# Optimization experiments

Measured on AMD Instinct MI355X. Metric: run time of the kernel, lower is better.

The kernel has to match this reference:

```python
import jax, jax.numpy as jnp
import numpy as np

K = 5          # init kwarg k: k-1 = 4 nearest neighbors used, randint over [0, k-2]
DIMS = 512     # init kwarg dims


def _pairwise_dist(X):
    # Faithful to find_k: euclidean distance matrix, computed via the
    # ||a||^2 + ||b||^2 - 2ab gram trick instead of the O(T) python loop.
    sq = jnp.sum(X * X, axis=1)
    d2 = sq[:, None] + sq[None, :] - 2.0 * (X @ X.T)
    return jnp.sqrt(jnp.maximum(d2, 0.0))


def _generate(min_samples, n_per, key):
    # SMOTE.generate: for each minority row, n_per synthetic samples, each
    # interpolated toward a uniformly chosen one of its k-1 nearest neighbors.
    T, d = min_samples.shape
    D = _pairwise_dist(min_samples)                       # [T, T]
    nbrs = jnp.argsort(D, axis=1)[:, 1:K]                 # [T, k-1], drop self
    k1, k2 = jax.random.split(key)
    choice = jax.random.randint(k1, (T, n_per), 0, K - 1)          # nn = randint(0, k-2)
    u = jax.random.uniform(k2, (T, n_per, 1), dtype=min_samples.dtype)  # uniform(0,1)
    nn_idx = jnp.take_along_axis(nbrs, choice, axis=1)    # [T, n_per]
    base = min_samples[:, None, :]                        # [T, 1, d]
    diff = min_samples[nn_idx] - base                     # [T, n_per, d]
    # populate() fills row-major (outer loop i, inner loop over N) -> reshape matches
    return (base + u * diff).reshape(T * n_per, d)


def setup_inputs() -> dict:
    key = jax.random.key(0)
    n_major, n_minor = 24576, 8192
    X = jax.random.normal(key, (n_major + n_minor, DIMS), dtype=jnp.float32)
    y = jnp.concatenate([jnp.zeros((n_major,), jnp.int32),
                         jnp.ones((n_minor,), jnp.int32)])
    return {"X": X, "y": y}


def reference(X, y):
    # forward: oversample every non-dominant class up to the dominant count.
    y_np = np.asarray(y)                       # labels are concrete constants
    occ = np.bincount(y_np)                    # == one_hot(y).sum(0)
    dom = int(occ.argmax())
    n_occ = int(occ[dom])
    key = jax.random.key(42)
    X_out = X
    y_out = y.astype(jnp.float32)
    for c in range(len(occ)):
        if c == dom:
            continue
        n_per = int((n_occ - int(occ[c])) * 100 / int(occ[c])) // 100  # int(N/100)
        if n_per <= 0:
            continue
        cand = X[y_np == c]
        key, sub = jax.random.split(key)
        xs = _generate(cand, n_per, sub)
        X_out = jnp.concatenate([X_out, xs], axis=0)
        y_out = jnp.concatenate([y_out, jnp.full((xs.shape[0],), float(c), jnp.float32)])
    return X_out, y_out
```

## Files before the change

kernel.cpp:

```cpp
#include <hip/hip_runtime.h>
#include <stdint.h>
#include <math.h>

#ifndef JAX_PARTITIONABLE
#define JAX_PARTITIONABLE 1
#endif

#define DIM    512
#define NTOT   32768
#define NMAJ   24576
#define NMIN   8192
#define NGEN   16384
#define XROWS  49152
#define Y_OFF  ((size_t)XROWS * DIM)

#define NSLICE 8
#define KSLICE 6
#define NCAND  (NSLICE * KSLICE)

#define WS_H       (NMIN)
#define WS_L       (WS_H + NMIN * DIM / 2)
#define WS_CAND_F  (WS_L + NMIN * DIM / 2)
#define WS_NBR_F   (WS_CAND_F + NMIN * NCAND / 2)

typedef __attribute__((ext_vector_type(8))) short bfv8;
typedef __attribute__((ext_vector_type(4))) float f32x4;

__device__ __forceinline__ void tf2x32(uint32_t k0, uint32_t k1,
                                       uint32_t x0, uint32_t x1,
                                       uint32_t &o0, uint32_t &o1) {
  const uint32_t ks2 = k0 ^ k1 ^ 0x1BD11BDAu;
  x0 += k0; x1 += k1;
#define TF_R(r) { x0 += x1; x1 = (x1 << (r)) | (x1 >> (32 - (r))); x1 ^= x0; }
  TF_R(13) TF_R(15) TF_R(26) TF_R(6)
  x0 += k1;  x1 += ks2 + 1u;
  TF_R(17) TF_R(29) TF_R(16) TF_R(24)
  x0 += ks2; x1 += k0 + 2u;
  TF_R(13) TF_R(15) TF_R(26) TF_R(6)
  x0 += k0;  x1 += k1 + 3u;
  TF_R(17) TF_R(29) TF_R(16) TF_R(24)
  x0 += k1;  x1 += ks2 + 4u;
  TF_R(13) TF_R(15) TF_R(26) TF_R(6)
  x0 += ks2; x1 += k0 + 5u;
#undef TF_R
  o0 = x0; o1 = x1;
}

#if JAX_PARTITIONABLE
__device__ __forceinline__ void jax_split(uint2 key, uint2 &c0, uint2 &c1) {
  tf2x32(key.x, key.y, 0u, 0u, c0.x, c0.y);
  tf2x32(key.x, key.y, 0u, 1u, c1.x, c1.y);
}
__device__ __forceinline__ uint32_t jax_bits(uint2 key, uint32_t f) {
  uint32_t a, b;
  tf2x32(key.x, key.y, 0u, f, a, b);
  return a ^ b;
}
#else
__device__ __forceinline__ void jax_split(uint2 key, uint2 &c0, uint2 &c1) {
  uint32_t a0, b0, a1, b1;
  tf2x32(key.x, key.y, 0u, 2u, a0, b0);
  tf2x32(key.x, key.y, 1u, 3u, a1, b1);
  c0 = make_uint2(a0, a1);
  c1 = make_uint2(b0, b1);
}
__device__ __forceinline__ uint32_t jax_bits(uint2 key, uint32_t f) {
  uint32_t a, b;
  if (f < (NGEN / 2)) { tf2x32(key.x, key.y, f, f + NGEN / 2, a, b); return a; }
  tf2x32(key.x, key.y, f - NGEN / 2, f, a, b); return b;
}
#endif

__device__ __forceinline__ void derive_keys(uint2 &k2, uint2 &k2i) {
  uint2 root = make_uint2(0u, 42u);
  uint2 dead, sub, k1;
  jax_split(root, dead, sub);
  jax_split(sub, k1, k2);
  jax_split(k1, dead, k2i);
}

__device__ __forceinline__ unsigned short f2bf(float x) {
  uint32_t u = __float_as_uint(x);
  uint32_t r = (u + 0x7FFFu + ((u >> 16) & 1u)) >> 16;
  return (unsigned short)r;
}

__global__ __launch_bounds__(256) void prep_kernel(const float* __restrict__ X,
                                                   float* __restrict__ wsf) {
  const int row  = blockIdx.x * 4 + (threadIdx.x >> 6);
  const int lane = threadIdx.x & 63;
  const float* Xm = X + (size_t)NMAJ * DIM;
  const float4* p = reinterpret_cast<const float4*>(Xm + (size_t)row * DIM);
  ushort4* H4 = reinterpret_cast<ushort4*>(wsf + WS_H) + (size_t)row * 128;
  double s = 0.0;
#pragma unroll
  for (int q = 0; q < 2; ++q) {
    float4 v = p[lane + q * 64];
    ushort4 h;
    h.x = f2bf(v.x); h.y = f2bf(v.y); h.z = f2bf(v.z); h.w = f2bf(v.w);
    H4[lane + q * 64] = h;
    s += (double)v.x * v.x + (double)v.y * v.y + (double)v.z * v.z + (double)v.w * v.w;
  }
#pragma unroll
  for (int off = 32; off > 0; off >>= 1) s += __shfl_down(s, off);
  if (lane == 0) wsf[row] = (float)s;
}

#define INSERT5B(TD, TI, dv, jv)                                           \
  { const bool b4 = (dv) < TD[4];                                          \
    if (__any(b4)) {                                                       \
      const bool b3 = (dv) < TD[3], b2 = (dv) < TD[2];                     \
      const bool b1 = (dv) < TD[1], b0 = (dv) < TD[0];                     \
      TD[4] = b3 ? TD[3] : (b4 ? (dv) : TD[4]);                            \
      TI[4] = b3 ? TI[3] : (b4 ? (jv) : TI[4]);                            \
      TD[3] = b2 ? TD[2] : (b3 ? (dv) : TD[3]);                            \
      TI[3] = b2 ? TI[2] : (b3 ? (jv) : TI[3]);                            \
      TD[2] = b1 ? TD[1] : (b2 ? (dv) : TD[2]);                            \
      TI[2] = b1 ? TI[1] : (b2 ? (jv) : TI[2]);                            \
      TD[1] = b0 ? TD[0] : (b1 ? (dv) : TD[1]);                            \
      TI[1] = b0 ? TI[0] : (b1 ? (jv) : TI[1]);                            \
      TD[0] = b0 ? (dv) : TD[0];                                           \
      TI[0] = b0 ? (jv) : TI[0];                                           \
    } }

__global__ __launch_bounds__(256, 2) void smote_main(float* wsf) {
  __shared__ __align__(16) char raw[3 * 24576];

  const unsigned short* Hm = reinterpret_cast<const unsigned short*>(wsf + WS_H);

  const int tid = threadIdx.x;
  const int w  = tid >> 6;
  const int l  = tid & 63;
  const int wm = w & 1;
  const int wn = w >> 1;
  const int lg = l >> 4;
  const int ll = l & 15;

  const int e  = blockIdx.x >> 6;
  const int n0 = (blockIdx.x & 63) * 128;

  const int csw = (lg ^ ((ll >> 1) & 3)) * 16;
  int aoff[4], boff[4];
#pragma unroll
  for (int f = 0; f < 4; ++f) {
    aoff[f] = (wm * 64 + f * 16 + ll) * 64 + csw;
    boff[f] = 16384 + (wn * 64 + f * 16 + ll) * 64 + csw;
  }

  const int srow   = l >> 2;
  const int schunk = ((l & 3) ^ ((l >> 3) & 3)) * 16;

  auto STAGE = [&](int cp2, int ks2, int bi) {
    char* buf = raw + bi * 24576;
    const int kb = ks2 * 64;
    const int jt = e * 1024 + cp2 * 256;
#pragma unroll
    for (int q = 0; q < 2; ++q) {
      const int rb = (q * 4 + w) * 16;
      const size_t roff = (size_t)(rb + srow) * 1024 + kb + schunk;
      const char* ga0 = (const char*)Hm + (size_t)jt * 1024 + roff;
      const char* ga1 = (const char*)Hm + (size_t)(jt + 128) * 1024 + roff;
      const char* gb  = (const char*)Hm + (size_t)n0 * 1024 + roff;
      __builtin_amdgcn_global_load_lds(
          (const __attribute__((address_space(1))) void*)ga0,
          (__attribute__((address_space(3))) void*)(buf + rb * 64), 16, 0, 0);
      __builtin_amdgcn_global_load_lds(
          (const __attribute__((address_space(1))) void*)ga1,
          (__attribute__((address_space(3))) void*)(buf + 8192 + rb * 64), 16, 0, 0);
      __builtin_amdgcn_global_load_lds(
          (const __attribute__((address_space(1))) void*)gb,
          (__attribute__((address_space(3))) void*)(buf + 16384 + rb * 64), 16, 0, 0);
    }
  };

  float td[4][5];
  int   ti_[4][5];
#pragma unroll
  for (int n = 0; n < 4; ++n)
#pragma unroll
    for (int s = 0; s < 5; ++s) { td[n][s] = 1e30f; ti_[n][s] = 0x7fffffff; }

  f32x4 accA[4][4], accB[4][4];
#pragma unroll
  for (int m = 0; m < 4; ++m)
#pragma unroll
    for (int n = 0; n < 4; ++n) {
      accA[m][n] = (f32x4){0.f, 0.f, 0.f, 0.f};
      accB[m][n] = (f32x4){0.f, 0.f, 0.f, 0.f};
    }

  STAGE(0, 0, 0);
  STAGE(0, 1, 1);

  int cur = 0;
  int ks = 0, cp = 0;
  int pks = 2, pcp = 0, pb = 2;

  for (int s = 0; s < 64; ++s) {
    asm volatile("s_waitcnt vmcnt(6)" ::: "memory");
    __builtin_amdgcn_s_barrier();
    __builtin_amdgcn_sched_barrier(0);

    STAGE(pcp, pks, pb);
    if (++pks == 16) { pks = 0; ++pcp; if (pcp == 4) pcp = 0; }
    if (++pb == 3) pb = 0;

    const char* buf = raw + cur * 24576;
    bfv8 bf[4], afA[4], afB[4];
#pragma unroll
    for (int n = 0; n < 4; ++n) bf[n]  = *reinterpret_cast<const bfv8*>(buf + boff[n]);
#pragma unroll
    for (int m = 0; m < 4; ++m) afA[m] = *reinterpret_cast<const bfv8*>(buf + aoff[m]);
#pragma unroll
    for (int m = 0; m < 4; ++m) afB[m] = *reinterpret_cast<const bfv8*>(buf + 8192 + aoff[m]);

    __builtin_amdgcn_s_setprio(1);
#pragma unroll
    for (int m = 0; m < 4; ++m)
#pragma unroll
      for (int n = 0; n < 4; ++n)
        accA[m][n] = __builtin_amdgcn_mfma_f32_16x16x32_bf16(afA[m], bf[n], accA[m][n], 0, 0, 0);
#pragma unroll
    for (int m = 0; m < 4; ++m)
#pragma unroll
      for (int n = 0; n < 4; ++n)
        accB[m][n] = __builtin_amdgcn_mfma_f32_16x16x32_bf16(afB[m], bf[n], accB[m][n], 0, 0, 0);
    __builtin_amdgcn_s_setprio(0);

    if (ks == 15) {
      const int jt = e * 1024 + cp * 256;
#pragma unroll
      for (int m = 0; m < 4; ++m) {
        const int jb = jt + wm * 64 + m * 16 + lg * 4;
        const float4 mj = *reinterpret_cast<const float4*>(&wsf[jb]);
        const float mjr[4] = {mj.x, mj.y, mj.z, mj.w};
#pragma unroll
        for (int r = 0; r < 4; ++r) {
#pragma unroll
          for (int n = 0; n < 4; ++n) {
            const float mv = mjr[r] - 2.0f * accA[m][n][r];
            INSERT5B(td[n], ti_[n], mv, jb + r);
          }
        }
      }
#pragma unroll
      for (int m = 0; m < 4; ++m) {
        const int jb = jt + 128 + wm * 64 + m * 16 + lg * 4;
        const float4 mj = *reinterpret_cast<const float4*>(&wsf[jb]);
        const float mjr[4] = {mj.x, mj.y, mj.z, mj.w};
#pragma unroll
        for (int r = 0; r < 4; ++r) {
#pragma unroll
          for (int n = 0; n < 4; ++n) {
            const float mv = mjr[r] - 2.0f * accB[m][n][r];
            INSERT5B(td[n], ti_[n], mv, jb + r);
          }
        }
      }
#pragma unroll
      for (int m = 0; m < 4; ++m)
#pragma unroll
        for (int n = 0; n < 4; ++n) {
          accA[m][n] = (f32x4){0.f, 0.f, 0.f, 0.f};
          accB[m][n] = (f32x4){0.f, 0.f, 0.f, 0.f};
        }
    }
    if (++ks == 16) { ks = 0; ++cp; }
    if (++cur == 3) cur = 0;
  }

  asm volatile("s_waitcnt vmcnt(0)" ::: "memory");
  __syncthreads();

  float* md = reinterpret_cast<float*>(raw);
  int*   mi = reinterpret_cast<int*>(raw + 20480);
  const int lid = wm * 4 + lg;
#pragma unroll
  for (int n = 0; n < 4; ++n) {
    const int col = wn * 64 + n * 16 + ll;
#pragma unroll
    for (int s = 0; s < 5; ++s) {
      md[(lid * 5 + s) * 128 + col] = td[n][s];
      mi[(lid * 5 + s) * 128 + col] = ti_[n][s];
    }
  }
  __syncthreads();
  if (tid < 128) {
    unsigned short* cand = reinterpret_cast<unsigned short*>(wsf + WS_CAND_F)
                         + (size_t)(n0 + tid) * NCAND + e * KSLICE;
    float ld = -1e31f; int li = -1;
    for (int s = 0; s < KSLICE; ++s) {
      float bd = 1e30f; int bi = 0x7fffffff;
      for (int c = 0; c < 40; ++c) {
        const float d = md[c * 128 + tid];
        const int  ix = mi[c * 128 + tid];
        const bool gt_last = (d > ld) || (d == ld && ix > li);
        const bool lt_best = (d < bd) || (d == bd && ix < bi);
        if (gt_last && lt_best) { bd = d; bi = ix; }
      }
      ld = bd; li = bi;
      cand[s] = (unsigned short)bi;
    }
  }
}

__global__ __launch_bounds__(256) void rerank_copy_kernel(const float* __restrict__ X,
                                                          const int* __restrict__ y,
                                                          float* __restrict__ wsf,
                                                          float* __restrict__ out) {
  const int bid = blockIdx.x;
  if ((bid & 1) == 0) {
    __shared__ unsigned long long keys_s[4][NCAND];
    const float* Xm = X + (size_t)NMAJ * DIM;
    const int wave = threadIdx.x >> 6;
    const int lane = threadIdx.x & 63;
    const int row  = (bid >> 1) * 4 + wave;

    const unsigned short* cand = reinterpret_cast<const unsigned short*>(wsf + WS_CAND_F)
                               + (size_t)row * NCAND;
    const float si = wsf[row];
    const float4* Xi = reinterpret_cast<const float4*>(Xm + (size_t)row * DIM);
    const float4 xi0 = Xi[lane], xi1 = Xi[lane + 64];

    const int jv = (lane < NCAND) ? (int)cand[lane] : 0;

#pragma unroll 4
    for (int c = 0; c < NCAND; ++c) {
      const int j = __shfl(jv, c);
      const float4* Xj = reinterpret_cast<const float4*>(Xm + (size_t)j * DIM);
      const float4 xj0 = Xj[lane], xj1 = Xj[lane + 64];
      double s = (double)xi0.x * xj0.x + (double)xi0.y * xj0.y
               + (double)xi0.z * xj0.z + (double)xi0.w * xj0.w
               + (double)xi1.x * xj1.x + (double)xi1.y * xj1.y
               + (double)xi1.z * xj1.z + (double)xi1.w * xj1.w;
#pragma unroll
      for (int off = 32; off > 0; off >>= 1) s += __shfl_down(s, off);
      if (lane == 0) {
        const float d2 = (si + wsf[j]) - 2.0f * (float)s;
        const float d  = (float)sqrt((double)fmaxf(d2, 0.0f));
        keys_s[wave][c] = ((unsigned long long)__float_as_uint(d) << 32) | (uint32_t)j;
      }
    }

    unsigned long long key = (lane < NCAND) ? keys_s[wave][lane] : ~0ull;
    int* nbr = reinterpret_cast<int*>(wsf) + WS_NBR_F + (size_t)row * 4;
#pragma unroll
    for (int s = 0; s < 5; ++s) {
      unsigned long long k = key;
#pragma unroll
      for (int off = 32; off > 0; off >>= 1) {
        const unsigned long long o = __shfl_xor(k, off);
        if (o < k) k = o;
      }
      if (key == k) key = ~0ull;
      if (s >= 1 && lane == 0) nbr[s - 1] = (int)(k & 0xffffffffu);
    }
  } else {
    const long long XF4 = (long long)NTOT * DIM / 4;
    const long long YF4 = XROWS / 4;
    long long idx = (long long)(bid >> 1) * 256 + threadIdx.x;
    const long long stride = (long long)(gridDim.x >> 1) * 256;
    for (long long i = idx; i < XF4 + YF4; i += stride) {
      if (i < XF4) {
        reinterpret_cast<float4*>(out)[i] = reinterpret_cast<const float4*>(X)[i];
      } else {
        long long j = i - XF4;
        float4 o;
        if (j < NTOT / 4) {
          int4 yv = reinterpret_cast<const int4*>(y)[j];
          o.x = (float)yv.x; o.y = (float)yv.y; o.z = (float)yv.z; o.w = (float)yv.w;
        } else {
          o.x = o.y = o.z = o.w = 1.0f;
        }
        reinterpret_cast<float4*>(out + Y_OFF)[j] = o;
      }
    }
  }
}

__global__ __launch_bounds__(256) void gen_kernel(const float* __restrict__ X,
                                                  const float* __restrict__ wsf,
                                                  float* __restrict__ out) {
  __shared__ int   nbr_s[32][4];
  __shared__ float u_s[64];
  __shared__ int   nb_s[64];
  const float* Xm = X + (size_t)NMAJ * DIM;
  const int r0 = blockIdx.x * 32;
  const int tid = threadIdx.x;

  if (tid < 32) {
    const int* nb = reinterpret_cast<const int*>(wsf) + WS_NBR_F + (size_t)(r0 + tid) * 4;
#pragma unroll
    for (int s = 0; s < 4; ++s) nbr_s[tid][s] = nb[s];
  }
  __syncthreads();
  if (tid < 64) {
    uint2 k2, k2i;
    derive_keys(k2, k2i);
    const uint32_t f = (uint32_t)(2 * r0 + tid);
    const uint32_t ch = jax_bits(k2i, f) & 3u;
    nb_s[tid] = nbr_s[tid >> 1][ch];
    const uint32_t ub = jax_bits(k2, f);
    u_s[tid] = __uint_as_float((ub >> 9) | 0x3f800000u) - 1.0f;
  }
  __syncthreads();

  const int c = tid * 2;
  for (int g = 0; g < 64; ++g) {
    const int i = g >> 1;
    const float u = u_s[g];
    const int nb = nb_s[g];
    float2 bv = *reinterpret_cast<const float2*>(Xm + (size_t)(r0 + i) * DIM + c);
    float2 nv = *reinterpret_cast<const float2*>(Xm + (size_t)nb * DIM + c);
    float2 o;
    o.x = bv.x + u * (nv.x - bv.x);
    o.y = bv.y + u * (nv.y - bv.y);
    *reinterpret_cast<float2*>(out + ((size_t)(NTOT + 2 * r0 + g)) * DIM + c) = o;
  }
}

extern "C" void kernel_launch(void* const* d_in, const int* in_sizes, int n_in,
                              void* d_out, int out_size, void* d_ws, size_t ws_size,
                              hipStream_t stream) {
  const float* X = (const float*)d_in[0];
  const int*   y = (const int*)d_in[1];
  float* out = (float*)d_out;
  float* wsf = (float*)d_ws;
  (void)in_sizes; (void)n_in; (void)out_size; (void)ws_size;

  prep_kernel       <<<dim3(NMIN / 4), dim3(256), 0, stream>>>(X, wsf);
  smote_main        <<<dim3(512),      dim3(256), 0, stream>>>(wsf);
  rerank_copy_kernel<<<dim3(4096),     dim3(256), 0, stream>>>(X, y, wsf, out);
  gen_kernel        <<<dim3(NMIN / 32), dim3(256), 0, stream>>>(X, wsf, out);
}
```

Baseline: 287.7 us.

## Fuse neighbor rerank with sample generation and split out the bulk copy

The exact-distance rerank of the candidate neighbors now feeds the interpolation in the same block. Selected neighbors stay in shared memory instead of making a global workspace round trip and needing a separate generation launch. The input/label copy moves into its own grid-stride kernel launched after. Generation now uses float4 accesses with one wave per pair of synthetic rows. The cost is that the copy no longer overlaps with the rerank inside one launch, and it adds a block-level sync in the rerank path.

```diff
diff --git a/kernel.cpp b/kernel.cpp
--- a/kernel.cpp
+++ b/kernel.cpp
@@ -21,7 +21,6 @@
 #define WS_H       (NMIN)
 #define WS_L       (WS_H + NMIN * DIM / 2)
 #define WS_CAND_F  (WS_L + NMIN * DIM / 2)
-#define WS_NBR_F   (WS_CAND_F + NMIN * NCAND / 2)
 
 typedef __attribute__((ext_vector_type(8))) short bfv8;
 typedef __attribute__((ext_vector_type(4))) float f32x4;
@@ -304,118 +303,111 @@
   }
 }
 
-__global__ __launch_bounds__(256) void rerank_copy_kernel(const float* __restrict__ X,
-                                                          const int* __restrict__ y,
-                                                          float* __restrict__ wsf,
-                                                          float* __restrict__ out) {
-  const int bid = blockIdx.x;
-  if ((bid & 1) == 0) {
-    __shared__ unsigned long long keys_s[4][NCAND];
-    const float* Xm = X + (size_t)NMAJ * DIM;
-    const int wave = threadIdx.x >> 6;
-    const int lane = threadIdx.x & 63;
-    const int row  = (bid >> 1) * 4 + wave;
-
-    const unsigned short* cand = reinterpret_cast<const unsigned short*>(wsf + WS_CAND_F)
-                               + (size_t)row * NCAND;
-    const float si = wsf[row];
-    const float4* Xi = reinterpret_cast<const float4*>(Xm + (size_t)row * DIM);
-    const float4 xi0 = Xi[lane], xi1 = Xi[lane + 64];
-
-    const int jv = (lane < NCAND) ? (int)cand[lane] : 0;
+__global__ __launch_bounds__(256) void rerank_gen_kernel(const float* __restrict__ X,
+                                                         float* __restrict__ wsf,
+                                                         float* __restrict__ out) {
+  __shared__ unsigned long long keys_s[4][NCAND];
+  __shared__ int   nbr_s[4][4];
+  __shared__ float u_s[8];
+  __shared__ int   nb_s[8];
+  const float* Xm = X + (size_t)NMAJ * DIM;
+  const int wave = threadIdx.x >> 6;
+  const int lane = threadIdx.x & 63;
+  const int r0b  = blockIdx.x * 4;
+  const int row  = r0b + wave;
+
+  const unsigned short* cand = reinterpret_cast<const unsigned short*>(wsf + WS_CAND_F)
+                             + (size_t)row * NCAND;
+  const float si = wsf[row];
+  const float4* Xi = reinterpret_cast<const float4*>(Xm + (size_t)row * DIM);
+  const float4 xi0 = Xi[lane], xi1 = Xi[lane + 64];
+
+  const int jv = (lane < NCAND) ? (int)cand[lane] : 0;
 
 #pragma unroll 4
-    for (int c = 0; c < NCAND; ++c) {
-      const int j = __shfl(jv, c);
-      const float4* Xj = reinterpret_cast<const float4*>(Xm + (size_t)j * DIM);
-      const float4 xj0 = Xj[lane], xj1 = Xj[lane + 64];
-      double s = (double)xi0.x * xj0.x + (double)xi0.y * xj0.y
-               + (double)xi0.z * xj0.z + (double)xi0.w * xj0.w
-               + (double)xi1.x * xj1.x + (double)xi1.y * xj1.y
-               + (double)xi1.z * xj1.z + (double)xi1.w * xj1.w;
-#pragma unroll
-      for (int off = 32; off > 0; off >>= 1) s += __shfl_down(s, off);
-      if (lane == 0) {
-        const float d2 = (si + wsf[j]) - 2.0f * (float)s;
-        const float d  = (float)sqrt((double)fmaxf(d2, 0.0f));
-        keys_s[wave][c] = ((unsigned long long)__float_as_uint(d) << 32) | (uint32_t)j;
-      }
-    }
-
-    unsigned long long key = (lane < NCAND) ? keys_s[wave][lane] : ~0ull;
-    int* nbr = reinterpret_cast<int*>(wsf) + WS_NBR_F + (size_t)row * 4;
-#pragma unroll
-    for (int s = 0; s < 5; ++s) {
-      unsigned long long k = key;
-#pragma unroll
-      for (int off = 32; off > 0; off >>= 1) {
-        const unsigned long long o = __shfl_xor(k, off);
-        if (o < k) k = o;
-      }
-      if (key == k) key = ~0ull;
-      if (s >= 1 && lane == 0) nbr[s - 1] = (int)(k & 0xffffffffu);
-    }
-  } else {
-    const long long XF4 = (long long)NTOT * DIM / 4;
-    const long long YF4 = XROWS / 4;
-    long long idx = (long long)(bid >> 1) * 256 + threadIdx.x;
-    const long long stride = (long long)(gridDim.x >> 1) * 256;
-    for (long long i = idx; i < XF4 + YF4; i += stride) {
-      if (i < XF4) {
-        reinterpret_cast<float4*>(out)[i] = reinterpret_cast<const float4*>(X)[i];
-      } else {
-        long long j = i - XF4;
-        float4 o;
-        if (j < NTOT / 4) {
-          int4 yv = reinterpret_cast<const int4*>(y)[j];
-          o.x = (float)yv.x; o.y = (float)yv.y; o.z = (float)yv.z; o.w = (float)yv.w;
-        } else {
-          o.x = o.y = o.z = o.w = 1.0f;
-        }
-        reinterpret_cast<float4*>(out + Y_OFF)[j] = o;
-      }
-    }
-  }
-}
-
-__global__ __launch_bounds__(256) void gen_kernel(const float* __restrict__ X,
-                                                  const float* __restrict__ wsf,
-                                                  float* __restrict__ out) {
-  __shared__ int   nbr_s[32][4];
-  __shared__ float u_s[64];
-  __shared__ int   nb_s[64];
-  const float* Xm = X + (size_t)NMAJ * DIM;
-  const int r0 = blockIdx.x * 32;
-  const int tid = threadIdx.x;
-
-  if (tid < 32) {
-    const int* nb = reinterpret_cast<const int*>(wsf) + WS_NBR_F + (size_t)(r0 + tid) * 4;
-#pragma unroll
-    for (int s = 0; s < 4; ++s) nbr_s[tid][s] = nb[s];
+  for (int c = 0; c < NCAND; ++c) {
+    const int j = __shfl(jv, c);
+    const float4* Xj = reinterpret_cast<const float4*>(Xm + (size_t)j * DIM);
+    const float4 xj0 = Xj[lane], xj1 = Xj[lane + 64];
+    double s = (double)xi0.x * xj0.x + (double)xi0.y * xj0.y
+             + (double)xi0.z * xj0.z + (double)xi0.w * xj0.w
+             + (double)xi1.x * xj1.x + (double)xi1.y * xj1.y
+             + (double)xi1.z * xj1.z + (double)xi1.w * xj1.w;
+#pragma unroll
+    for (int off = 32; off > 0; off >>= 1) s += __shfl_down(s, off);
+    if (lane == 0) {
+      const float d2 = (si + wsf[j]) - 2.0f * (float)s;
+      const float d  = (float)sqrt((double)fmaxf(d2, 0.0f));
+      keys_s[wave][c] = ((unsigned long long)__float_as_uint(d) << 32) | (uint32_t)j;
+    }
+  }
+
+  unsigned long long key = (lane < NCAND) ? keys_s[wave][lane] : ~0ull;
+#pragma unroll
+  for (int s = 0; s < 5; ++s) {
+    unsigned long long k = key;
+#pragma unroll
+    for (int off = 32; off > 0; off >>= 1) {
+      const unsigned long long o = __shfl_xor(k, off);
+      if (o < k) k = o;
+    }
+    if (key == k) key = ~0ull;
+    if (s >= 1 && lane == 0) nbr_s[wave][s - 1] = (int)(k & 0xffffffffu);
   }
   __syncthreads();
-  if (tid < 64) {
+
+  if (threadIdx.x < 8) {
     uint2 k2, k2i;
     derive_keys(k2, k2i);
-    const uint32_t f = (uint32_t)(2 * r0 + tid);
+    const uint32_t f = (uint32_t)(2 * r0b + threadIdx.x);
     const uint32_t ch = jax_bits(k2i, f) & 3u;
-    nb_s[tid] = nbr_s[tid >> 1][ch];
+    nb_s[threadIdx.x] = nbr_s[threadIdx.x >> 1][ch];
     const uint32_t ub = jax_bits(k2, f);
-    u_s[tid] = __uint_as_float((ub >> 9) | 0x3f800000u) - 1.0f;
+    u_s[threadIdx.x] = __uint_as_float((ub >> 9) | 0x3f800000u) - 1.0f;
   }
   __syncthreads();
 
-  const int c = tid * 2;
-  for (int g = 0; g < 64; ++g) {
-    const int i = g >> 1;
-    const float u = u_s[g];
-    const int nb = nb_s[g];
-    float2 bv = *reinterpret_cast<const float2*>(Xm + (size_t)(r0 + i) * DIM + c);
-    float2 nv = *reinterpret_cast<const float2*>(Xm + (size_t)nb * DIM + c);
-    float2 o;
-    o.x = bv.x + u * (nv.x - bv.x);
-    o.y = bv.y + u * (nv.y - bv.y);
-    *reinterpret_cast<float2*>(out + ((size_t)(NTOT + 2 * r0 + g)) * DIM + c) = o;
+  const int g  = threadIdx.x >> 5;
+  const int cb = (threadIdx.x & 31) * 16;
+  const float u = u_s[g];
+  const int  nb = nb_s[g];
+  const int  ai = r0b + (g >> 1);
+  const float4* bp = reinterpret_cast<const float4*>(Xm + (size_t)ai * DIM + cb);
+  const float4* np = reinterpret_cast<const float4*>(Xm + (size_t)nb * DIM + cb);
+  float4* op = reinterpret_cast<float4*>(out + (size_t)(NTOT + 2 * r0b + g) * DIM + cb);
+#pragma unroll
+  for (int q = 0; q < 4; ++q) {
+    const float4 b = bp[q], nv = np[q];
+    float4 o;
+    o.x = b.x + u * (nv.x - b.x);
+    o.y = b.y + u * (nv.y - b.y);
+    o.z = b.z + u * (nv.z - b.z);
+    o.w = b.w + u * (nv.w - b.w);
+    op[q] = o;
+  }
+}
+
+__global__ __launch_bounds__(256) void copy_kernel(const float* __restrict__ X,
+                                                   const int* __restrict__ y,
+                                                   float* __restrict__ out) {
+  const long long XF4 = (long long)NTOT * DIM / 4;
+  const long long YF4 = XROWS / 4;
+  long long idx = (long long)blockIdx.x * blockDim.x + threadIdx.x;
+  const long long stride = (long long)gridDim.x * blockDim.x;
+  for (long long i = idx; i < XF4 + YF4; i += stride) {
+    if (i < XF4) {
+      reinterpret_cast<float4*>(out)[i] = reinterpret_cast<const float4*>(X)[i];
+    } else {
+      long long j = i - XF4;
+      float4 o;
+      if (j < NTOT / 4) {
+        int4 yv = reinterpret_cast<const int4*>(y)[j];
+        o.x = (float)yv.x; o.y = (float)yv.y; o.z = (float)yv.z; o.w = (float)yv.w;
+      } else {
+        o.x = o.y = o.z = o.w = 1.0f;
+      }
+      reinterpret_cast<float4*>(out + Y_OFF)[j] = o;
+    }
   }
 }
 
@@ -428,8 +420,8 @@
   float* wsf = (float*)d_ws;
   (void)in_sizes; (void)n_in; (void)out_size; (void)ws_size;
 
-  prep_kernel       <<<dim3(NMIN / 4), dim3(256), 0, stream>>>(X, wsf);
-  smote_main        <<<dim3(512),      dim3(256), 0, stream>>>(wsf);
-  rerank_copy_kernel<<<dim3(4096),     dim3(256), 0, stream>>>(X, y, wsf, out);
-  gen_kernel        <<<dim3(NMIN / 32), dim3(256), 0, stream>>>(X, wsf, out);
-}
+  prep_kernel      <<<dim3(NMIN / 4), dim3(256), 0, stream>>>(X, wsf);
+  smote_main       <<<dim3(512),      dim3(256), 0, stream>>>(wsf);
+  rerank_gen_kernel<<<dim3(NMIN / 4), dim3(256), 0, stream>>>(X, wsf, out);
+  copy_kernel      <<<dim3(2048),     dim3(256), 0, stream>>>(X, y, out);
+}
```

After: 240.6 us. 16.4% less time.
